# Optimization experiments

Measured on AMD Instinct MI355X. Metric: run time of the kernel, lower is better.

Reference implementation:

```python
import jax, jax.numpy as jnp
import numpy as np

H = 1024        # hidden_dim
MD = 2048       # memory_dim
L = 16384       # memory length == max_length
N = 8           # head_N
# sys.float_info.min underflows to 0.0 in float32, exactly as in the torch
# original (python float * float32 tensor). Kept for faithfulness.
TINY = jnp.float32(2.2250738585072014e-308)


def setup_inputs() -> dict:
    key = jax.random.key(0)
    ks = jax.random.split(key, 12)
    s_h = 1.0 / np.sqrt(H)
    s_m = 1.0 / np.sqrt(MD)
    s_o = 1.0 / np.sqrt(2 * H)
    return {
        "x": jax.random.normal(ks[0], (1, 1, H), jnp.float32),
        "memory": jax.random.normal(ks[1], (L, MD), jnp.float32),
        "Wq": jax.random.uniform(ks[2], (H, H), jnp.float32, -s_h, s_h),
        "bq": jax.random.uniform(ks[3], (H,), jnp.float32, -s_h, s_h),
        "Wk": jax.random.uniform(ks[4], (H, MD), jnp.float32, -s_m, s_m),
        "bk": jax.random.uniform(ks[5], (H,), jnp.float32, -s_m, s_m),
        "Wv": jax.random.uniform(ks[6], (H, MD), jnp.float32, -s_m, s_m),
        "bv": jax.random.uniform(ks[7], (H,), jnp.float32, -s_m, s_m),
        "Wo": jax.random.uniform(ks[8], (H, 2 * H), jnp.float32, -s_o, s_o),
        "bo": jax.random.uniform(ks[9], (H,), jnp.float32, -s_o, s_o),
    }


def reference(x, memory, Wq, bq, Wk, bk, Wv, bv, Wo, bo):
    d = H // N  # per-head dim
    # Q: (1,H) -> (1,d,N) -> (N,1,d), scaled by d**-0.5
    q = x.reshape(1, -1) @ Wq.T + bq
    Q = q.reshape(1, d, N).transpose(2, 0, 1) * (d ** -0.5)
    # K: (L,H) -> (L,d,N) -> (N,d,L)
    K = (memory @ Wk.T + bk).reshape(-1, d, N).transpose(2, 1, 0)
    QK = jnp.einsum('nod,ndl->nol', Q, K)  # (N,1,L)
    # pad mask: 1 where the memory row sums to zero, else 0 (as in torch nonzero-set)
    any_zero = memory.sum(axis=1)
    pad_mask = (any_zero == 0).astype(QK.dtype)[None, None, :]
    QK = QK + pad_mask * TINY
    attn = jax.nn.softmax(QK, axis=-1)
    # V: (L,H) -> (L,d,N) -> (N,L,d)
    V = (memory @ Wv.T + bv).reshape(-1, d, N).transpose(2, 0, 1)
    feat = jnp.einsum('nol,nld->nod', attn, V)      # (N,1,d)
    feat = feat.transpose(1, 2, 0).reshape(1, 1, H)  # (1,1,H)
    ax = jnp.concatenate([x, feat], axis=-1)         # (1,1,2H)
    return jax.nn.relu(ax @ Wo.T + bo)
```

## Files before the change

### kernel.cpp

```cpp
#include <hip/hip_runtime.h>
#include <math.h>

#define LROWS 16384
#define HDIM  1024
#define MDIM  2048
#define NH    8
#define RSQRT_D 0.08838834764831844f

#define OFF_W     0
#define OFF_BETA  16384
#define OFF_Z     16392
#define OFF_Y     16400
#define OFF_SMAX  32784
#define OFF_Q     32792
#define OFF_FEAT  33816
#define OFF_S     34840
#define OFF_P     165912

__device__ __forceinline__ float dot4(float4 a, float4 b) {
  return a.x * b.x + a.y * b.y + a.z * b.z + a.w * b.w;
}
__device__ __forceinline__ void fma4(float4& acc, float s, float4 v) {
  acc.x = fmaf(s, v.x, acc.x); acc.y = fmaf(s, v.y, acc.y);
  acc.z = fmaf(s, v.z, acc.z); acc.w = fmaf(s, v.w, acc.w);
}

__device__ void atomicMaxF(float* addr, float v) {
  int* ai = (int*)addr;
  int old = __float_as_int(-3.4e38f);
  while (v > __int_as_float(old)) {
    int assumed = old;
    old = atomicCAS(ai, assumed, __float_as_int(v));
    if (old == assumed) break;
  }
}

__global__ __launch_bounds__(256) void k1_q(const float* __restrict__ x,
                                            const float* __restrict__ Wq,
                                            const float* __restrict__ bq,
                                            const float* __restrict__ bk,
                                            float* __restrict__ ws) {
  int tid = threadIdx.x, lane = tid & 63;
  int j = blockIdx.x * 4 + (tid >> 6);
  const float4* xr = (const float4*)x;
  const float4* wr = (const float4*)(Wq + (size_t)j * HDIM);
  float acc = 0.f;
#pragma unroll
  for (int i = 0; i < 4; ++i) {
    int idx = i * 64 + lane;
    acc += dot4(xr[idx], wr[idx]);
  }
#pragma unroll
  for (int off = 32; off; off >>= 1) acc += __shfl_xor(acc, off);
  if (lane == 0) {
    float qj = acc + bq[j];
    ws[OFF_Q + j] = qj;
    atomicAdd(&ws[OFF_BETA + (j & 7)], qj * bk[j]);
  }
}

__global__ __launch_bounds__(256) void k2_w(const float* __restrict__ Wk,
                                            float* __restrict__ ws) {
  int tid = threadIdx.x;
  int mc = blockIdx.x & 7, cc = blockIdx.x >> 3;
  int m = mc * 256 + tid;
  const float* q = ws + OFF_Q;
  float acc[8];
#pragma unroll
  for (int n = 0; n < 8; ++n) acc[n] = 0.f;
  int c0 = cc * 64;
  for (int c = c0; c < c0 + 64; c += 8) {
#pragma unroll
    for (int u = 0; u < 8; ++u)
      acc[u] = fmaf(q[c + u], Wk[(size_t)(c + u) * MDIM + m], acc[u]);
  }
#pragma unroll
  for (int n = 0; n < 8; ++n) atomicAdd(&ws[OFF_W + n * MDIM + m], acc[n]);
}

__global__ __launch_bounds__(256) void k3_s(const float* __restrict__ mem,
                                            float* __restrict__ ws) {
  __shared__ float sred[256 * 36];
  __shared__ float redmax[2][8];
  int tid = threadIdx.x, lane = tid & 63, wv = tid >> 6;
  int r0 = blockIdx.x * 16 + wv * 4;
  const float* wmat = ws + OFF_W;
  float acc[4][8];
#pragma unroll
  for (int rr = 0; rr < 4; ++rr)
#pragma unroll
    for (int n = 0; n < 8; ++n) acc[rr][n] = 0.f;

  for (int step = 0; step < 8; ++step) {
    int mq = step * 64 + lane;
    float4 wvv[8];
#pragma unroll
    for (int n = 0; n < 8; ++n)
      wvv[n] = *(const float4*)(wmat + n * MDIM + mq * 4);
#pragma unroll
    for (int rr = 0; rr < 4; ++rr) {
      float4 mv = *(const float4*)(mem + (size_t)(r0 + rr) * MDIM + mq * 4);
#pragma unroll
      for (int n = 0; n < 8; ++n) {
        acc[rr][n] = fmaf(mv.x, wvv[n].x, acc[rr][n]);
        acc[rr][n] = fmaf(mv.y, wvv[n].y, acc[rr][n]);
        acc[rr][n] = fmaf(mv.z, wvv[n].z, acc[rr][n]);
        acc[rr][n] = fmaf(mv.w, wvv[n].w, acc[rr][n]);
      }
    }
  }
#pragma unroll
  for (int rr = 0; rr < 4; ++rr)
#pragma unroll
    for (int n = 0; n < 8; ++n)
      sred[tid * 36 + rr * 8 + n] = acc[rr][n];
  __syncthreads();

  if (tid < 128) {
    int rowl = tid >> 3, n = tid & 7;
    int wvx = rowl >> 2, rr = rowl & 3;
    const float* base = sred + (wvx * 64) * 36 + rr * 8 + n;
    float s = 0.f;
#pragma unroll
    for (int l = 0; l < 64; ++l) s += base[l * 36];
    s = (s + ws[OFF_BETA + n]) * RSQRT_D;
    int r = blockIdx.x * 16 + rowl;
    ws[OFF_S + (size_t)r * 8 + n] = s;
    float mx = s;
    mx = fmaxf(mx, __shfl_xor(mx, 8));
    mx = fmaxf(mx, __shfl_xor(mx, 16));
    mx = fmaxf(mx, __shfl_xor(mx, 32));
    if (lane < 8) redmax[tid >> 6][lane] = mx;
  }
  __syncthreads();
  if (tid < 8) atomicMaxF(&ws[OFF_SMAX + tid], fmaxf(redmax[0][tid], redmax[1][tid]));
}

__global__ __launch_bounds__(256) void k4_p(float* __restrict__ ws) {
  int r = blockIdx.x * 256 + threadIdx.x;
  const float4* srow = (const float4*)(ws + OFF_S + (size_t)r * 8);
  float4 mx0 = *(const float4*)(ws + OFF_SMAX);
  float4 mx1 = *(const float4*)(ws + OFF_SMAX + 4);
  float4 s0 = srow[0], s1 = srow[1];
  float4 e0, e1;
  e0.x = __expf(s0.x - mx0.x); e0.y = __expf(s0.y - mx0.y);
  e0.z = __expf(s0.z - mx0.z); e0.w = __expf(s0.w - mx0.w);
  e1.x = __expf(s1.x - mx1.x); e1.y = __expf(s1.y - mx1.y);
  e1.z = __expf(s1.z - mx1.z); e1.w = __expf(s1.w - mx1.w);
  float4* prow = (float4*)(ws + OFF_P + (size_t)r * 8);
  prow[0] = e0; prow[1] = e1;
#pragma unroll
  for (int off = 32; off; off >>= 1) {
    e0.x += __shfl_xor(e0.x, off); e0.y += __shfl_xor(e0.y, off);
    e0.z += __shfl_xor(e0.z, off); e0.w += __shfl_xor(e0.w, off);
    e1.x += __shfl_xor(e1.x, off); e1.y += __shfl_xor(e1.y, off);
    e1.z += __shfl_xor(e1.z, off); e1.w += __shfl_xor(e1.w, off);
  }
  if ((threadIdx.x & 63) == 0) {
    atomicAdd(&ws[OFF_Z + 0], e0.x); atomicAdd(&ws[OFF_Z + 1], e0.y);
    atomicAdd(&ws[OFF_Z + 2], e0.z); atomicAdd(&ws[OFF_Z + 3], e0.w);
    atomicAdd(&ws[OFF_Z + 4], e1.x); atomicAdd(&ws[OFF_Z + 5], e1.y);
    atomicAdd(&ws[OFF_Z + 6], e1.z); atomicAdd(&ws[OFF_Z + 7], e1.w);
  }
}

__global__ __launch_bounds__(256) void k5_y(const float* __restrict__ mem,
                                            float* __restrict__ ws) {
  __shared__ float4 sred[2048];
  int tid = threadIdx.x;
  int cb = blockIdx.x & 15, rc = blockIdx.x >> 4;
  int mq = cb * 32 + (tid & 31);
  int ro = tid >> 5;
  const float4* pbase = (const float4*)(ws + OFF_P);
  float4 acc[8];
#pragma unroll
  for (int n = 0; n < 8; ++n) acc[n] = make_float4(0.f, 0.f, 0.f, 0.f);
  for (int i = 0; i < 64; ++i) {
    int r = rc * 512 + i * 8 + ro;
    float4 mv = *(const float4*)(mem + (size_t)r * MDIM + mq * 4);
    float4 p0 = pbase[(size_t)r * 2];
    float4 p1 = pbase[(size_t)r * 2 + 1];
    fma4(acc[0], p0.x, mv); fma4(acc[1], p0.y, mv);
    fma4(acc[2], p0.z, mv); fma4(acc[3], p0.w, mv);
    fma4(acc[4], p1.x, mv); fma4(acc[5], p1.y, mv);
    fma4(acc[6], p1.z, mv); fma4(acc[7], p1.w, mv);
  }
#pragma unroll
  for (int n = 0; n < 8; ++n) sred[n * 256 + ro * 32 + (tid & 31)] = acc[n];
  __syncthreads();
  {
    int n = tid >> 5, ml = tid & 31;
    float4 s = sred[n * 256 + ml];
#pragma unroll
    for (int r2 = 1; r2 < 8; ++r2) {
      float4 v = sred[n * 256 + r2 * 32 + ml];
      s.x += v.x; s.y += v.y; s.z += v.z; s.w += v.w;
    }
    float* yb = ws + OFF_Y + n * MDIM + cb * 128 + ml * 4;
    atomicAdd(yb + 0, s.x); atomicAdd(yb + 1, s.y);
    atomicAdd(yb + 2, s.z); atomicAdd(yb + 3, s.w);
  }
}

__global__ __launch_bounds__(256) void k6_feat(const float* __restrict__ Wv,
                                               const float* __restrict__ bv,
                                               float* __restrict__ ws) {
  int tid = threadIdx.x, lane = tid & 63;
  int c = blockIdx.x * 4 + (tid >> 6);
  int n = c & 7;
  const float4* yb = (const float4*)(ws + OFF_Y + n * MDIM);
  const float4* wb = (const float4*)(Wv + (size_t)c * MDIM);
  float acc = 0.f;
#pragma unroll
  for (int s = 0; s < 8; ++s) {
    int idx = s * 64 + lane;
    acc += dot4(yb[idx], wb[idx]);
  }
#pragma unroll
  for (int off = 32; off; off >>= 1) acc += __shfl_xor(acc, off);
  if (lane == 0) ws[OFF_FEAT + c] = acc / ws[OFF_Z + n] + bv[c];
}

__global__ __launch_bounds__(256) void k7_out(const float* __restrict__ x,
                                              const float* __restrict__ Wo,
                                              const float* __restrict__ bo,
                                              const float* __restrict__ ws,
                                              float* __restrict__ out) {
  int tid = threadIdx.x, lane = tid & 63;
  int j = blockIdx.x * 4 + (tid >> 6);
  const float4* wb = (const float4*)(Wo + (size_t)j * 2048);
  const float4* xr = (const float4*)x;
  const float4* fr = (const float4*)(ws + OFF_FEAT);
  float acc = 0.f;
#pragma unroll
  for (int s = 0; s < 4; ++s) {
    int idx = s * 64 + lane;
    acc += dot4(xr[idx], wb[idx]);
    acc += dot4(fr[idx], wb[256 + idx]);
  }
#pragma unroll
  for (int off = 32; off; off >>= 1) acc += __shfl_xor(acc, off);
  if (lane == 0) out[j] = fmaxf(acc + bo[j], 0.f);
}

extern "C" void kernel_launch(void* const* d_in, const int* in_sizes, int n_in,
                              void* d_out, int out_size, void* d_ws, size_t ws_size,
                              hipStream_t stream) {
  const float* x   = (const float*)d_in[0];
  const float* mem = (const float*)d_in[1];
  const float* Wq  = (const float*)d_in[2];
  const float* bq  = (const float*)d_in[3];
  const float* Wk  = (const float*)d_in[4];
  const float* bk  = (const float*)d_in[5];
  const float* Wv  = (const float*)d_in[6];
  const float* bv  = (const float*)d_in[7];
  const float* Wo  = (const float*)d_in[8];
  const float* bo  = (const float*)d_in[9];
  float* ws  = (float*)d_ws;
  float* out = (float*)d_out;

  hipMemsetAsync(ws, 0, OFF_SMAX * sizeof(float), stream);
  hipMemsetAsync(ws + OFF_SMAX, 0xFE, 8 * sizeof(float), stream);

  k1_q   <<<256,  256, 0, stream>>>(x, Wq, bq, bk, ws);
  k2_w   <<<128,  256, 0, stream>>>(Wk, ws);
  k3_s   <<<1024, 256, 0, stream>>>(mem, ws);
  k4_p   <<<64,   256, 0, stream>>>(ws);
  k5_y   <<<512,  256, 0, stream>>>(mem, ws);
  k6_feat<<<256,  256, 0, stream>>>(Wv, bv, ws);
  k7_out <<<256,  256, 0, stream>>>(x, Wo, bo, ws, out);
}
```

Measured before the change: 311.8 us.

## Fuse softmax exp into weighted-sum kernel and drop separate pass

```diff
diff --git a/kernel.cpp b/kernel.cpp
--- a/kernel.cpp
+++ b/kernel.cpp
@@ -15,7 +15,6 @@
 #define OFF_Q     32792
 #define OFF_FEAT  33816
 #define OFF_S     34840
-#define OFF_P     165912
 
 __device__ __forceinline__ float dot4(float4 a, float4 b) {
   return a.x * b.x + a.y * b.y + a.z * b.z + a.w * b.w;
@@ -41,6 +40,7 @@
                                             const float* __restrict__ bk,
                                             float* __restrict__ ws) {
   int tid = threadIdx.x, lane = tid & 63;
+  if (blockIdx.x == 0 && tid < 8) ws[OFF_SMAX + tid] = -3.4e38f;
   int j = blockIdx.x * 4 + (tid >> 6);
   const float4* xr = (const float4*)x;
   const float4* wr = (const float4*)(Wq + (size_t)j * HDIM);
@@ -80,7 +80,7 @@
 
 __global__ __launch_bounds__(256) void k3_s(const float* __restrict__ mem,
                                             float* __restrict__ ws) {
-  __shared__ float sred[256 * 36];
+  __shared__ float sred[4 * 32 * 33];
   __shared__ float redmax[2][8];
   int tid = threadIdx.x, lane = tid & 63, wv = tid >> 6;
   int r0 = blockIdx.x * 16 + wv * 4;
@@ -112,17 +112,23 @@
 #pragma unroll
   for (int rr = 0; rr < 4; ++rr)
 #pragma unroll
-    for (int n = 0; n < 8; ++n)
-      sred[tid * 36 + rr * 8 + n] = acc[rr][n];
+    for (int n = 0; n < 8; ++n) acc[rr][n] += __shfl_xor(acc[rr][n], 32);
+  if (lane < 32) {
+#pragma unroll
+    for (int rr = 0; rr < 4; ++rr)
+#pragma unroll
+      for (int n = 0; n < 8; ++n)
+        sred[wv * 1056 + lane * 33 + rr * 8 + n] = acc[rr][n];
+  }
   __syncthreads();
 
   if (tid < 128) {
     int rowl = tid >> 3, n = tid & 7;
     int wvx = rowl >> 2, rr = rowl & 3;
-    const float* base = sred + (wvx * 64) * 36 + rr * 8 + n;
+    const float* base = sred + wvx * 1056 + rr * 8 + n;
     float s = 0.f;
 #pragma unroll
-    for (int l = 0; l < 64; ++l) s += base[l * 36];
+    for (int l = 0; l < 32; ++l) s += base[l * 33];
     s = (s + ws[OFF_BETA + n]) * RSQRT_D;
     int r = blockIdx.x * 16 + rowl;
     ws[OFF_S + (size_t)r * 8 + n] = s;
@@ -136,64 +142,76 @@
   if (tid < 8) atomicMaxF(&ws[OFF_SMAX + tid], fmaxf(redmax[0][tid], redmax[1][tid]));
 }
 
-__global__ __launch_bounds__(256) void k4_p(float* __restrict__ ws) {
-  int r = blockIdx.x * 256 + threadIdx.x;
-  const float4* srow = (const float4*)(ws + OFF_S + (size_t)r * 8);
-  float4 mx0 = *(const float4*)(ws + OFF_SMAX);
-  float4 mx1 = *(const float4*)(ws + OFF_SMAX + 4);
-  float4 s0 = srow[0], s1 = srow[1];
-  float4 e0, e1;
-  e0.x = __expf(s0.x - mx0.x); e0.y = __expf(s0.y - mx0.y);
-  e0.z = __expf(s0.z - mx0.z); e0.w = __expf(s0.w - mx0.w);
-  e1.x = __expf(s1.x - mx1.x); e1.y = __expf(s1.y - mx1.y);
-  e1.z = __expf(s1.z - mx1.z); e1.w = __expf(s1.w - mx1.w);
-  float4* prow = (float4*)(ws + OFF_P + (size_t)r * 8);
-  prow[0] = e0; prow[1] = e1;
-#pragma unroll
-  for (int off = 32; off; off >>= 1) {
-    e0.x += __shfl_xor(e0.x, off); e0.y += __shfl_xor(e0.y, off);
-    e0.z += __shfl_xor(e0.z, off); e0.w += __shfl_xor(e0.w, off);
-    e1.x += __shfl_xor(e1.x, off); e1.y += __shfl_xor(e1.y, off);
-    e1.z += __shfl_xor(e1.z, off); e1.w += __shfl_xor(e1.w, off);
-  }
-  if ((threadIdx.x & 63) == 0) {
-    atomicAdd(&ws[OFF_Z + 0], e0.x); atomicAdd(&ws[OFF_Z + 1], e0.y);
-    atomicAdd(&ws[OFF_Z + 2], e0.z); atomicAdd(&ws[OFF_Z + 3], e0.w);
-    atomicAdd(&ws[OFF_Z + 4], e1.x); atomicAdd(&ws[OFF_Z + 5], e1.y);
-    atomicAdd(&ws[OFF_Z + 6], e1.z); atomicAdd(&ws[OFF_Z + 7], e1.w);
-  }
-}
-
 __global__ __launch_bounds__(256) void k5_y(const float* __restrict__ mem,
                                             float* __restrict__ ws) {
-  __shared__ float4 sred[2048];
+  __shared__ float pLds[256 * 8];
+  __shared__ float4 sred[4 * 8 * 32];
   int tid = threadIdx.x;
   int cb = blockIdx.x & 15, rc = blockIdx.x >> 4;
+  int r0 = rc * 256;
+  {
+    const float4* srow = (const float4*)(ws + OFF_S + (size_t)(r0 + tid) * 8);
+    float4 mx0 = *(const float4*)(ws + OFF_SMAX);
+    float4 mx1 = *(const float4*)(ws + OFF_SMAX + 4);
+    float4 s0 = srow[0], s1 = srow[1];
+    float4 e0, e1;
+    e0.x = __expf(s0.x - mx0.x); e0.y = __expf(s0.y - mx0.y);
+    e0.z = __expf(s0.z - mx0.z); e0.w = __expf(s0.w - mx0.w);
+    e1.x = __expf(s1.x - mx1.x); e1.y = __expf(s1.y - mx1.y);
+    e1.z = __expf(s1.z - mx1.z); e1.w = __expf(s1.w - mx1.w);
+    ((float4*)pLds)[tid * 2] = e0;
+    ((float4*)pLds)[tid * 2 + 1] = e1;
+    if (cb == 0) {
+      float v0x = e0.x, v0y = e0.y, v0z = e0.z, v0w = e0.w;
+      float v1x = e1.x, v1y = e1.y, v1z = e1.z, v1w = e1.w;
+#pragma unroll
+      for (int off = 32; off; off >>= 1) {
+        v0x += __shfl_xor(v0x, off); v0y += __shfl_xor(v0y, off);
+        v0z += __shfl_xor(v0z, off); v0w += __shfl_xor(v0w, off);
+        v1x += __shfl_xor(v1x, off); v1y += __shfl_xor(v1y, off);
+        v1z += __shfl_xor(v1z, off); v1w += __shfl_xor(v1w, off);
+      }
+      if ((tid & 63) == 0) {
+        atomicAdd(&ws[OFF_Z + 0], v0x); atomicAdd(&ws[OFF_Z + 1], v0y);
+        atomicAdd(&ws[OFF_Z + 2], v0z); atomicAdd(&ws[OFF_Z + 3], v0w);
+        atomicAdd(&ws[OFF_Z + 4], v1x); atomicAdd(&ws[OFF_Z + 5], v1y);
+        atomicAdd(&ws[OFF_Z + 6], v1z); atomicAdd(&ws[OFF_Z + 7], v1w);
+      }
+    }
+  }
+  __syncthreads();
   int mq = cb * 32 + (tid & 31);
   int ro = tid >> 5;
-  const float4* pbase = (const float4*)(ws + OFF_P);
   float4 acc[8];
 #pragma unroll
   for (int n = 0; n < 8; ++n) acc[n] = make_float4(0.f, 0.f, 0.f, 0.f);
-  for (int i = 0; i < 64; ++i) {
-    int r = rc * 512 + i * 8 + ro;
-    float4 mv = *(const float4*)(mem + (size_t)r * MDIM + mq * 4);
-    float4 p0 = pbase[(size_t)r * 2];
-    float4 p1 = pbase[(size_t)r * 2 + 1];
+  for (int i = 0; i < 32; ++i) {
+    int rl = i * 8 + ro;
+    float4 mv = *(const float4*)(mem + (size_t)(r0 + rl) * MDIM + mq * 4);
+    float4 p0 = ((const float4*)pLds)[rl * 2];
+    float4 p1 = ((const float4*)pLds)[rl * 2 + 1];
     fma4(acc[0], p0.x, mv); fma4(acc[1], p0.y, mv);
     fma4(acc[2], p0.z, mv); fma4(acc[3], p0.w, mv);
     fma4(acc[4], p1.x, mv); fma4(acc[5], p1.y, mv);
     fma4(acc[6], p1.z, mv); fma4(acc[7], p1.w, mv);
   }
-#pragma unroll
-  for (int n = 0; n < 8; ++n) sred[n * 256 + ro * 32 + (tid & 31)] = acc[n];
+  int lane = tid & 63, w = tid >> 6;
+#pragma unroll
+  for (int n = 0; n < 8; ++n) {
+    acc[n].x += __shfl_xor(acc[n].x, 32); acc[n].y += __shfl_xor(acc[n].y, 32);
+    acc[n].z += __shfl_xor(acc[n].z, 32); acc[n].w += __shfl_xor(acc[n].w, 32);
+  }
+  if (lane < 32) {
+#pragma unroll
+    for (int n = 0; n < 8; ++n) sred[(w * 8 + n) * 32 + lane] = acc[n];
+  }
   __syncthreads();
   {
     int n = tid >> 5, ml = tid & 31;
-    float4 s = sred[n * 256 + ml];
-#pragma unroll
-    for (int r2 = 1; r2 < 8; ++r2) {
-      float4 v = sred[n * 256 + r2 * 32 + ml];
+    float4 s = sred[n * 32 + ml];
+#pragma unroll
+    for (int w2 = 1; w2 < 4; ++w2) {
+      float4 v = sred[(w2 * 8 + n) * 32 + ml];
       s.x += v.x; s.y += v.y; s.z += v.z; s.w += v.w;
     }
     float* yb = ws + OFF_Y + n * MDIM + cb * 128 + ml * 4;
@@ -260,13 +278,11 @@
   float* out = (float*)d_out;
 
   hipMemsetAsync(ws, 0, OFF_SMAX * sizeof(float), stream);
-  hipMemsetAsync(ws + OFF_SMAX, 0xFE, 8 * sizeof(float), stream);
 
   k1_q   <<<256,  256, 0, stream>>>(x, Wq, bq, bk, ws);
   k2_w   <<<128,  256, 0, stream>>>(Wk, ws);
   k3_s   <<<1024, 256, 0, stream>>>(mem, ws);
-  k4_p   <<<64,   256, 0, stream>>>(ws);
-  k5_y   <<<512,  256, 0, stream>>>(mem, ws);
+  k5_y   <<<1024, 256, 0, stream>>>(mem, ws);
   k6_feat<<<256,  256, 0, stream>>>(Wv, bv, ws);
   k7_out <<<256,  256, 0, stream>>>(x, Wo, bo, ws, out);
 }
```

Result: no change. 310.6 us (-0.4%).
